# Optimization experiments

Hardware: AMD Instinct MI355X
Metric: run time of the kernel (lower is better)

The kernel has to match this reference:

```python
import jax, jax.numpy as jnp
import numpy as np

EPS = 1e-6
NUM_HEADS = 4


def setup_inputs() -> dict:
    key = jax.random.key(0)
    ks = jax.random.split(key, 7)
    B, C, H, W = 4, 128, 64, 64
    x = jax.random.normal(ks[0], (B, C, H, W), dtype=jnp.float32)
    norm_w = jnp.ones((C,), dtype=jnp.float32)
    norm_b = jnp.zeros((C,), dtype=jnp.float32)
    # 1x1 convs stored as [out_ch, in_ch] matrices
    qkv_w = jax.random.normal(ks[1], (3 * C, C), dtype=jnp.float32) / np.sqrt(C)
    qkv_b = jnp.zeros((3 * C,), dtype=jnp.float32)
    proj_w = jax.random.normal(ks[2], (C, C), dtype=jnp.float32) / np.sqrt(C)
    proj_b = jnp.zeros((C,), dtype=jnp.float32)
    return {"x": x, "norm_w": norm_w, "norm_b": norm_b,
            "qkv_w": qkv_w, "qkv_b": qkv_b, "proj_w": proj_w, "proj_b": proj_b}


def reference(x, norm_w, norm_b, qkv_w, qkv_b, proj_w, proj_b):
    B, C, H, W = x.shape
    nh = NUM_HEADS
    dh = C // nh
    N = H * W

    # ChannelLayerNorm: stats over channel dim per spatial position
    mean = jnp.mean(x, axis=1, keepdims=True)
    var = jnp.mean(jnp.square(x - mean), axis=1, keepdims=True)  # unbiased=False
    h = (x - mean) * jax.lax.rsqrt(var + EPS)
    h = h * norm_w[None, :, None, None] + norm_b[None, :, None, None]

    # qkv 1x1 conv -> [B, 3C, H, W]
    qkv = jnp.einsum('oc,bchw->bohw', qkv_w, h) + qkv_b[None, :, None, None]
    qkv = qkv.reshape(B, 3, nh, dh, N)
    q, k, v = qkv[:, 0], qkv[:, 1], qkv[:, 2]  # each [B, nh, dh, N]

    scale = dh ** -0.5
    attn = jnp.einsum('bhcn,bhcm->bhnm', q, k) * scale  # [B, nh, N, N]
    attn = jax.nn.softmax(attn, axis=-1)
    h = jnp.einsum('bhnm,bhcm->bhcn', attn, v)  # [B, nh, dh, N]
    h = h.reshape(B, C, H, W)

    h = jnp.einsum('oc,bchw->bohw', proj_w, h) + proj_b[None, :, None, None]
    return x + h
```

## Files before the change

### kernel.cpp

```cpp
#include <hip/hip_runtime.h>
#include <hip/hip_bf16.h>
#include <math.h>

#define BB 4
#define CC 128
#define NH 4
#define DH 32
#define NN 4096
#define OC3 (3*CC)

typedef __attribute__((ext_vector_type(8))) short short8;
typedef __attribute__((ext_vector_type(4))) short short4v;
typedef __attribute__((ext_vector_type(4))) float float4v;

__device__ inline short f2bf(float f) {
    unsigned u = __builtin_bit_cast(unsigned, f);
    u += 0x7FFF + ((u >> 16) & 1);
    return (short)(u >> 16);
}
__device__ inline unsigned pk2bf(float a, float b) {
    __hip_bfloat162 h = __float22bfloat162_rn(make_float2(a, b));
    unsigned u; __builtin_memcpy(&u, &h, 4);
    return u;
}

__global__ __launch_bounds__(256) void wcvt_kernel(
        const float* __restrict__ qw, const float* __restrict__ pw,
        short* __restrict__ wb) {
    int i = (blockIdx.x * 256 + threadIdx.x) * 8;
    const float* src = (i < OC3 * CC) ? (qw + i) : (pw + (i - OC3 * CC));
    float4 f0 = *(const float4*)(src);
    float4 f1 = *(const float4*)(src + 4);
    union { short8 v; unsigned u[4]; } z;
    z.u[0] = pk2bf(f0.x, f0.y); z.u[1] = pk2bf(f0.z, f0.w);
    z.u[2] = pk2bf(f1.x, f1.y); z.u[3] = pk2bf(f1.z, f1.w);
    *(short8*)(wb + i) = z.v;
}

#define HS 136
__global__ __launch_bounds__(512, 4) void lnqkv_kernel(
        const float* __restrict__ x, const float* __restrict__ nw,
        const float* __restrict__ nb, const short* __restrict__ qwb,
        const float* __restrict__ qbias,
        short* __restrict__ qT, short* __restrict__ kT, short* __restrict__ vv) {
    __shared__ short hT[64 * HS];
    __shared__ float red[16][64];
    __shared__ float mrs[2][64];
    int t = threadIdx.x;
    int n0g = blockIdx.x * 64;
    int b = n0g >> 12, n0 = n0g & (NN - 1);
    int nl = t & 63, cq = t >> 6;

    const float* xp = x + ((size_t)b * CC + cq * 16) * NN + n0 + nl;
    float xv[16];
    float s = 0.f, ss = 0.f;
    #pragma unroll
    for (int j = 0; j < 16; ++j) {
        xv[j] = xp[(size_t)j * NN];
        s += xv[j]; ss += xv[j] * xv[j];
    }
    red[cq][nl] = s; red[cq + 8][nl] = ss;
    __syncthreads();
    if (t < 64) {
        float s8 = 0.f, q8 = 0.f;
        #pragma unroll
        for (int j = 0; j < 8; ++j) { s8 += red[j][t]; q8 += red[j + 8][t]; }
        float mean = s8 * (1.0f / CC);
        float var  = q8 * (1.0f / CC) - mean * mean;
        mrs[0][t] = mean;
        mrs[1][t] = rsqrtf(var + 1e-6f);
    }
    __syncthreads();
    {
        float mean = mrs[0][nl], rsv = mrs[1][nl];
        #pragma unroll
        for (int j = 0; j < 16; j += 8) {
            union { short8 v; unsigned u[4]; } z;
            #pragma unroll
            for (int k = 0; k < 4; ++k) {
                int c = cq * 16 + j + 2 * k;
                float h0 = (xv[j + 2 * k]     - mean) * rsv * nw[c]     + nb[c];
                float h1 = (xv[j + 2 * k + 1] - mean) * rsv * nw[c + 1] + nb[c + 1];
                z.u[k] = pk2bf(h0, h1);
            }
            *(short8*)&hT[nl * HS + cq * 16 + j] = z.v;
        }
    }
    __syncthreads();

    int w = t >> 6, lane = t & 63;
    int lg = lane >> 4, ln = lane & 15;
    #pragma unroll
    for (int it = 0; it < 3; ++it) {
        int ow = (w + it * 8) * 16;
        const short* wp = qwb + (size_t)(ow + ln) * CC;
        float4v a0 = {0,0,0,0}, a1 = {0,0,0,0}, a2 = {0,0,0,0}, a3 = {0,0,0,0};
        #pragma unroll
        for (int cs = 0; cs < 4; ++cs) {
            short8 af = *(const short8*)(wp + cs * 32 + lg * 8);
            const short* hp = &hT[cs * 32 + lg * 8];
            a0 = __builtin_amdgcn_mfma_f32_16x16x32_bf16(af, *(const short8*)&hp[(0  + ln) * HS], a0, 0, 0, 0);
            a1 = __builtin_amdgcn_mfma_f32_16x16x32_bf16(af, *(const short8*)&hp[(16 + ln) * HS], a1, 0, 0, 0);
            a2 = __builtin_amdgcn_mfma_f32_16x16x32_bf16(af, *(const short8*)&hp[(32 + ln) * HS], a2, 0, 0, 0);
            a3 = __builtin_amdgcn_mfma_f32_16x16x32_bf16(af, *(const short8*)&hp[(48 + ln) * HS], a3, 0, 0, 0);
        }
        int r0 = ow + lg * 4;
        float b0 = qbias[r0], b1 = qbias[r0 + 1], b2 = qbias[r0 + 2], b3 = qbias[r0 + 3];
        int cb = ow & 31;
        float4v* accs[4] = {&a0, &a1, &a2, &a3};
        if (it == 0) {
            const float qs = 0.1767766952966369f * 1.4426950408889634f;
            int hh = ow >> 5;
            size_t rowbase = (size_t)(b * NH + hh) * NN + n0;
            #pragma unroll
            for (int nsub = 0; nsub < 4; ++nsub) {
                float4v av = *accs[nsub];
                union { short4v v; unsigned u[2]; } z;
                z.u[0] = pk2bf((av.x + b0) * qs, (av.y + b1) * qs);
                z.u[1] = pk2bf((av.z + b2) * qs, (av.w + b3) * qs);
                *(short4v*)&qT[(rowbase + nsub * 16 + ln) * DH + cb + lg * 4] = z.v;
            }
        } else if (it == 1) {
            int hh = (ow - CC) >> 5;
            size_t rowbase = (size_t)(b * NH + hh) * NN + n0;
            #pragma unroll
            for (int nsub = 0; nsub < 4; ++nsub) {
                float4v av = *accs[nsub];
                union { short4v v; unsigned u[2]; } z;
                z.u[0] = pk2bf(av.x + b0, av.y + b1);
                z.u[1] = pk2bf(av.z + b2, av.w + b3);
                *(short4v*)&kT[(rowbase + nsub * 16 + ln) * DH + cb + lg * 4] = z.v;
            }
        } else {
            int hh = (ow - 2 * CC) >> 5;
            size_t cbase = (size_t)((b * NH + hh) * DH + cb + lg * 4);
            #pragma unroll
            for (int nsub = 0; nsub < 4; ++nsub) {
                float4v av = *accs[nsub];
                size_t col = (size_t)n0 + nsub * 16 + ln;
                vv[(cbase + 0) * NN + col] = f2bf(av.x + b0);
                vv[(cbase + 1) * NN + col] = f2bf(av.y + b1);
                vv[(cbase + 2) * NN + col] = f2bf(av.z + b2);
                vv[(cbase + 3) * NN + col] = f2bf(av.w + b3);
            }
        }
    }
}

#define PS 72
union __align__(16) FlashSh {
    short pt[8 * 16 * PS];
    struct { float mo[3][8][64][8]; float ml[3][8][64]; } m;
};
__global__ __launch_bounds__(512, 2) void flash_kernel(
        const short* __restrict__ qT, const short* __restrict__ kT,
        const short* __restrict__ vv, short* __restrict__ aoT) {
    __shared__ FlashSh sh;
    int blk = blockIdx.x;
    int bh = blk >> 5;
    int qb = blk & 31;
    int b = bh >> 2, hh = bh & 3;
    int n0 = qb * 128;
    int t = threadIdx.x, w = t >> 6, lane = t & 63;
    int lg = lane >> 4, ln = lane & 15;
    int qg = w & 1;
    int split = w >> 1;

    const short* kbase = kT + (size_t)bh * NN * DH + lg * 8;
    const short* vb0 = vv + ((size_t)bh * DH + ln) * NN + lg * 8;
    const short* vb1 = vb0 + (size_t)16 * NN;

    short8 qf[4];
    #pragma unroll
    for (int j = 0; j < 4; ++j)
        qf[j] = *(const short8*)&qT[((size_t)bh * NN + n0 + (qg * 4 + j) * 16 + ln) * DH + lg * 8];

    union { short8 v; unsigned u[4]; } onesf;
    onesf.u[0] = 0x3F803F80u; onesf.u[1] = 0x3F803F80u;
    onesf.u[2] = 0x3F803F80u; onesf.u[3] = 0x3F803F80u;

    float4v o0[4], o1[4], sacc[4];
    #pragma unroll
    for (int j = 0; j < 4; ++j) {
        o0[j] = (float4v){0,0,0,0}; o1[j] = (float4v){0,0,0,0};
        sacc[j] = (float4v){0,0,0,0};
    }
    short* ptw = &sh.pt[w * 16 * PS];

    int mbeg = split * (NN / 4), mend = mbeg + NN / 4;
    for (int m0 = mbeg; m0 < mend; m0 += 64) {
        const short* kp = kbase + (size_t)m0 * DH;
        short8 k0 = *(const short8*)(kp + (size_t)(ln +  0) * DH);
        short8 k1 = *(const short8*)(kp + (size_t)(ln + 16) * DH);
        short8 k2 = *(const short8*)(kp + (size_t)(ln + 32) * DH);
        short8 k3 = *(const short8*)(kp + (size_t)(ln + 48) * DH);
        short8 v0 = *(const short8*)(vb0 + m0);
        short8 v1 = *(const short8*)(vb0 + m0 + 32);
        short8 v2 = *(const short8*)(vb1 + m0);
        short8 v3 = *(const short8*)(vb1 + m0 + 32);

        #pragma unroll
        for (int j = 0; j < 4; ++j) {
            float4v s0 = {0,0,0,0}, s1 = s0, s2 = s0, s3 = s0;
            s0 = __builtin_amdgcn_mfma_f32_16x16x32_bf16(k0, qf[j], s0, 0, 0, 0);
            s1 = __builtin_amdgcn_mfma_f32_16x16x32_bf16(k1, qf[j], s1, 0, 0, 0);
            s2 = __builtin_amdgcn_mfma_f32_16x16x32_bf16(k2, qf[j], s2, 0, 0, 0);
            s3 = __builtin_amdgcn_mfma_f32_16x16x32_bf16(k3, qf[j], s3, 0, 0, 0);
            float4v* sv[4] = {&s0, &s1, &s2, &s3};
            #pragma unroll
            for (int jj = 0; jj < 4; ++jj) {
                float4v sj = *sv[jj];
                float p0 = __builtin_amdgcn_exp2f(sj.x);
                float p1 = __builtin_amdgcn_exp2f(sj.y);
                float p2 = __builtin_amdgcn_exp2f(sj.z);
                float p3 = __builtin_amdgcn_exp2f(sj.w);
                union { short4v v; unsigned u[2]; } z;
                z.u[0] = pk2bf(p0, p1); z.u[1] = pk2bf(p2, p3);
                *(short4v*)&ptw[ln * PS + jj * 16 + lg * 4] = z.v;
            }
            short8 pb0 = *(const short8*)&ptw[ln * PS + 0  + lg * 8];
            short8 pb1 = *(const short8*)&ptw[ln * PS + 32 + lg * 8];
            o0[j]   = __builtin_amdgcn_mfma_f32_16x16x32_bf16(v0, pb0, o0[j], 0, 0, 0);
            o1[j]   = __builtin_amdgcn_mfma_f32_16x16x32_bf16(v2, pb0, o1[j], 0, 0, 0);
            sacc[j] = __builtin_amdgcn_mfma_f32_16x16x32_bf16(onesf.v, pb0, sacc[j], 0, 0, 0);
            o0[j]   = __builtin_amdgcn_mfma_f32_16x16x32_bf16(v1, pb1, o0[j], 0, 0, 0);
            o1[j]   = __builtin_amdgcn_mfma_f32_16x16x32_bf16(v3, pb1, o1[j], 0, 0, 0);
            sacc[j] = __builtin_amdgcn_mfma_f32_16x16x32_bf16(onesf.v, pb1, sacc[j], 0, 0, 0);
        }
    }

    float ls[4];
    #pragma unroll
    for (int j = 0; j < 4; ++j) ls[j] = sacc[j].x;

    __syncthreads();
    if (split > 0) {
        int si = split - 1;
        #pragma unroll
        for (int j = 0; j < 4; ++j) {
            int tid = qg * 4 + j;
            float* mp = &sh.m.mo[si][tid][lane][0];
            *(float4*)(mp + 0) = make_float4(o0[j].x, o0[j].y, o0[j].z, o0[j].w);
            *(float4*)(mp + 4) = make_float4(o1[j].x, o1[j].y, o1[j].z, o1[j].w);
            sh.m.ml[si][tid][lane] = ls[j];
        }
    }
    __syncthreads();
    if (split == 0) {
        #pragma unroll
        for (int j = 0; j < 4; ++j) {
            int tid = qg * 4 + j;
            #pragma unroll
            for (int si = 0; si < 3; ++si) {
                const float* mp = &sh.m.mo[si][tid][lane][0];
                float4 a0 = *(const float4*)(mp + 0);
                float4 a1 = *(const float4*)(mp + 4);
                o0[j].x += a0.x; o0[j].y += a0.y; o0[j].z += a0.z; o0[j].w += a0.w;
                o1[j].x += a1.x; o1[j].y += a1.y; o1[j].z += a1.z; o1[j].w += a1.w;
                ls[j] += sh.m.ml[si][tid][lane];
            }
            float inv = 1.0f / ls[j];
            short* ap = aoT + ((size_t)b * NN + n0 + tid * 16 + ln) * CC + hh * DH;
            union { short4v v; unsigned u[2]; } z;
            z.u[0] = pk2bf(o0[j].x * inv, o0[j].y * inv);
            z.u[1] = pk2bf(o0[j].z * inv, o0[j].w * inv);
            *(short4v*)&ap[lg * 4] = z.v;
            z.u[0] = pk2bf(o1[j].x * inv, o1[j].y * inv);
            z.u[1] = pk2bf(o1[j].z * inv, o1[j].w * inv);
            *(short4v*)&ap[16 + lg * 4] = z.v;
        }
    }
}

__global__ __launch_bounds__(256) void proj_kernel(
        const short* __restrict__ aoT, const short* __restrict__ pwb,
        const float* __restrict__ pb, const float* __restrict__ x,
        float* __restrict__ out) {
    int t = threadIdx.x;
    int n0g = blockIdx.x * 64;
    int b = n0g >> 12, n0 = n0g & (NN - 1);
    int o0 = blockIdx.y * 64;
    int wo = t >> 6, lane = t & 63;
    int lg = lane >> 4, ln = lane & 15;
    int ow = o0 + wo * 16;
    const short* wp = pwb + (size_t)(ow + ln) * CC;
    const short* ap = aoT + (size_t)n0g * CC + lg * 8;
    float4v a0 = {0,0,0,0}, a1 = {0,0,0,0}, a2 = {0,0,0,0}, a3 = {0,0,0,0};
    #pragma unroll
    for (int cs = 0; cs < 4; ++cs) {
        short8 af = *(const short8*)(wp + cs * 32 + lg * 8);
        const short* hp = ap + cs * 32;
        a0 = __builtin_amdgcn_mfma_f32_16x16x32_bf16(af, *(const short8*)&hp[(size_t)(0  + ln) * CC], a0, 0, 0, 0);
        a1 = __builtin_amdgcn_mfma_f32_16x16x32_bf16(af, *(const short8*)&hp[(size_t)(16 + ln) * CC], a1, 0, 0, 0);
        a2 = __builtin_amdgcn_mfma_f32_16x16x32_bf16(af, *(const short8*)&hp[(size_t)(32 + ln) * CC], a2, 0, 0, 0);
        a3 = __builtin_amdgcn_mfma_f32_16x16x32_bf16(af, *(const short8*)&hp[(size_t)(48 + ln) * CC], a3, 0, 0, 0);
    }
    int r0 = ow + lg * 4;
    float b0 = pb[r0], b1 = pb[r0 + 1], b2 = pb[r0 + 2], b3 = pb[r0 + 3];
    const float* xbase = x   + ((size_t)b * CC + r0) * NN + n0 + ln;
    float*       obase = out + ((size_t)b * CC + r0) * NN + n0 + ln;
    float4v* accs[4] = {&a0, &a1, &a2, &a3};
    #pragma unroll
    for (int nsub = 0; nsub < 4; ++nsub) {
        float4v av = *accs[nsub];
        const float* xp = xbase + nsub * 16;
        float* op = obase + nsub * 16;
        op[(size_t)0 * NN] = av.x + b0 + xp[(size_t)0 * NN];
        op[(size_t)1 * NN] = av.y + b1 + xp[(size_t)1 * NN];
        op[(size_t)2 * NN] = av.z + b2 + xp[(size_t)2 * NN];
        op[(size_t)3 * NN] = av.w + b3 + xp[(size_t)3 * NN];
    }
}

extern "C" void kernel_launch(void* const* d_in, const int* in_sizes, int n_in,
                              void* d_out, int out_size, void* d_ws, size_t ws_size,
                              hipStream_t stream) {
    const float* x    = (const float*)d_in[0];
    const float* nw   = (const float*)d_in[1];
    const float* nb   = (const float*)d_in[2];
    const float* qkvw = (const float*)d_in[3];
    const float* qkvb = (const float*)d_in[4];
    const float* pw   = (const float*)d_in[5];
    const float* pb   = (const float*)d_in[6];
    float* out = (float*)d_out;

    short* qT  = (short*)d_ws;
    short* kT  = qT + (size_t)BB * NH * NN * DH;
    short* vv  = kT + (size_t)BB * NH * NN * DH;
    short* aoT = vv + (size_t)BB * NH * DH * NN;
    short* wb  = aoT + (size_t)BB * NH * DH * NN;
    short* qwb = wb;
    short* pwb = wb + (size_t)OC3 * CC;

    wcvt_kernel<<<dim3(32), 256, 0, stream>>>(qkvw, pw, wb);
    lnqkv_kernel<<<dim3(256), 512, 0, stream>>>(x, nw, nb, qwb, qkvb, qT, kT, vv);
    flash_kernel<<<dim3(512), 512, 0, stream>>>(qT, kT, vv, aoT);
    proj_kernel<<<dim3(256, 2), 256, 0, stream>>>(aoT, pwb, pb, x, out);
}
```

Measured before the change: 153.5 us.

## Halve LN/proj tiles, prefetch K/V in flash loop, sum softmax denominators in VALU

New measurement: 153.5 us. Within noise of the previous version (-0.0%).

```diff
diff --git a/kernel.cpp b/kernel.cpp
--- a/kernel.cpp
+++ b/kernel.cpp
@@ -43,28 +43,28 @@
         const float* __restrict__ nb, const short* __restrict__ qwb,
         const float* __restrict__ qbias,
         short* __restrict__ qT, short* __restrict__ kT, short* __restrict__ vv) {
-    __shared__ short hT[64 * HS];
-    __shared__ float red[16][64];
-    __shared__ float mrs[2][64];
+    __shared__ short hT[32 * HS];
+    __shared__ float red[2][16][32];
+    __shared__ float mrs[2][32];
     int t = threadIdx.x;
-    int n0g = blockIdx.x * 64;
+    int n0g = blockIdx.x * 32;
     int b = n0g >> 12, n0 = n0g & (NN - 1);
-    int nl = t & 63, cq = t >> 6;
-
-    const float* xp = x + ((size_t)b * CC + cq * 16) * NN + n0 + nl;
-    float xv[16];
+    int nl = t & 31, cq = t >> 5;
+
+    const float* xp = x + ((size_t)b * CC + cq * 8) * NN + n0 + nl;
+    float xv[8];
     float s = 0.f, ss = 0.f;
     #pragma unroll
-    for (int j = 0; j < 16; ++j) {
+    for (int j = 0; j < 8; ++j) {
         xv[j] = xp[(size_t)j * NN];
         s += xv[j]; ss += xv[j] * xv[j];
     }
-    red[cq][nl] = s; red[cq + 8][nl] = ss;
-    __syncthreads();
-    if (t < 64) {
+    red[0][cq][nl] = s; red[1][cq][nl] = ss;
+    __syncthreads();
+    if (t < 32) {
         float s8 = 0.f, q8 = 0.f;
         #pragma unroll
-        for (int j = 0; j < 8; ++j) { s8 += red[j][t]; q8 += red[j + 8][t]; }
+        for (int j = 0; j < 16; ++j) { s8 += red[0][j][t]; q8 += red[1][j][t]; }
         float mean = s8 * (1.0f / CC);
         float var  = q8 * (1.0f / CC) - mean * mean;
         mrs[0][t] = mean;
@@ -73,18 +73,15 @@
     __syncthreads();
     {
         float mean = mrs[0][nl], rsv = mrs[1][nl];
-        #pragma unroll
-        for (int j = 0; j < 16; j += 8) {
-            union { short8 v; unsigned u[4]; } z;
-            #pragma unroll
-            for (int k = 0; k < 4; ++k) {
-                int c = cq * 16 + j + 2 * k;
-                float h0 = (xv[j + 2 * k]     - mean) * rsv * nw[c]     + nb[c];
-                float h1 = (xv[j + 2 * k + 1] - mean) * rsv * nw[c + 1] + nb[c + 1];
-                z.u[k] = pk2bf(h0, h1);
-            }
-            *(short8*)&hT[nl * HS + cq * 16 + j] = z.v;
-        }
+        union { short8 v; unsigned u[4]; } z;
+        #pragma unroll
+        for (int k = 0; k < 4; ++k) {
+            int c = cq * 8 + 2 * k;
+            float h0 = (xv[2 * k]     - mean) * rsv * nw[c]     + nb[c];
+            float h1 = (xv[2 * k + 1] - mean) * rsv * nw[c + 1] + nb[c + 1];
+            z.u[k] = pk2bf(h0, h1);
+        }
+        *(short8*)&hT[nl * HS + cq * 8] = z.v;
     }
     __syncthreads();
 
@@ -94,26 +91,24 @@
     for (int it = 0; it < 3; ++it) {
         int ow = (w + it * 8) * 16;
         const short* wp = qwb + (size_t)(ow + ln) * CC;
-        float4v a0 = {0,0,0,0}, a1 = {0,0,0,0}, a2 = {0,0,0,0}, a3 = {0,0,0,0};
+        float4v a0 = {0,0,0,0}, a1 = {0,0,0,0};
         #pragma unroll
         for (int cs = 0; cs < 4; ++cs) {
             short8 af = *(const short8*)(wp + cs * 32 + lg * 8);
             const short* hp = &hT[cs * 32 + lg * 8];
             a0 = __builtin_amdgcn_mfma_f32_16x16x32_bf16(af, *(const short8*)&hp[(0  + ln) * HS], a0, 0, 0, 0);
             a1 = __builtin_amdgcn_mfma_f32_16x16x32_bf16(af, *(const short8*)&hp[(16 + ln) * HS], a1, 0, 0, 0);
-            a2 = __builtin_amdgcn_mfma_f32_16x16x32_bf16(af, *(const short8*)&hp[(32 + ln) * HS], a2, 0, 0, 0);
-            a3 = __builtin_amdgcn_mfma_f32_16x16x32_bf16(af, *(const short8*)&hp[(48 + ln) * HS], a3, 0, 0, 0);
         }
         int r0 = ow + lg * 4;
         float b0 = qbias[r0], b1 = qbias[r0 + 1], b2 = qbias[r0 + 2], b3 = qbias[r0 + 3];
         int cb = ow & 31;
-        float4v* accs[4] = {&a0, &a1, &a2, &a3};
+        float4v* accs[2] = {&a0, &a1};
         if (it == 0) {
             const float qs = 0.1767766952966369f * 1.4426950408889634f;
             int hh = ow >> 5;
             size_t rowbase = (size_t)(b * NH + hh) * NN + n0;
             #pragma unroll
-            for (int nsub = 0; nsub < 4; ++nsub) {
+            for (int nsub = 0; nsub < 2; ++nsub) {
                 float4v av = *accs[nsub];
                 union { short4v v; unsigned u[2]; } z;
                 z.u[0] = pk2bf((av.x + b0) * qs, (av.y + b1) * qs);
@@ -124,7 +119,7 @@
             int hh = (ow - CC) >> 5;
             size_t rowbase = (size_t)(b * NH + hh) * NN + n0;
             #pragma unroll
-            for (int nsub = 0; nsub < 4; ++nsub) {
+            for (int nsub = 0; nsub < 2; ++nsub) {
                 float4v av = *accs[nsub];
                 union { short4v v; unsigned u[2]; } z;
                 z.u[0] = pk2bf(av.x + b0, av.y + b1);
@@ -135,7 +130,7 @@
             int hh = (ow - 2 * CC) >> 5;
             size_t cbase = (size_t)((b * NH + hh) * DH + cb + lg * 4);
             #pragma unroll
-            for (int nsub = 0; nsub < 4; ++nsub) {
+            for (int nsub = 0; nsub < 2; ++nsub) {
                 float4v av = *accs[nsub];
                 size_t col = (size_t)n0 + nsub * 16 + ln;
                 vv[(cbase + 0) * NN + col] = f2bf(av.x + b0);
@@ -175,29 +170,37 @@
     for (int j = 0; j < 4; ++j)
         qf[j] = *(const short8*)&qT[((size_t)bh * NN + n0 + (qg * 4 + j) * 16 + ln) * DH + lg * 8];
 
-    union { short8 v; unsigned u[4]; } onesf;
-    onesf.u[0] = 0x3F803F80u; onesf.u[1] = 0x3F803F80u;
-    onesf.u[2] = 0x3F803F80u; onesf.u[3] = 0x3F803F80u;
-
-    float4v o0[4], o1[4], sacc[4];
+    float4v o0[4], o1[4];
+    float ls[4];
     #pragma unroll
     for (int j = 0; j < 4; ++j) {
-        o0[j] = (float4v){0,0,0,0}; o1[j] = (float4v){0,0,0,0};
-        sacc[j] = (float4v){0,0,0,0};
+        o0[j] = (float4v){0,0,0,0}; o1[j] = (float4v){0,0,0,0}; ls[j] = 0.f;
     }
     short* ptw = &sh.pt[w * 16 * PS];
 
     int mbeg = split * (NN / 4), mend = mbeg + NN / 4;
+
+    const short* kp0 = kbase + (size_t)mbeg * DH;
+    short8 k0 = *(const short8*)(kp0 + (size_t)(ln +  0) * DH);
+    short8 k1 = *(const short8*)(kp0 + (size_t)(ln + 16) * DH);
+    short8 k2 = *(const short8*)(kp0 + (size_t)(ln + 32) * DH);
+    short8 k3 = *(const short8*)(kp0 + (size_t)(ln + 48) * DH);
+    short8 v0 = *(const short8*)(vb0 + mbeg);
+    short8 v1 = *(const short8*)(vb0 + mbeg + 32);
+    short8 v2 = *(const short8*)(vb1 + mbeg);
+    short8 v3 = *(const short8*)(vb1 + mbeg + 32);
+
     for (int m0 = mbeg; m0 < mend; m0 += 64) {
-        const short* kp = kbase + (size_t)m0 * DH;
-        short8 k0 = *(const short8*)(kp + (size_t)(ln +  0) * DH);
-        short8 k1 = *(const short8*)(kp + (size_t)(ln + 16) * DH);
-        short8 k2 = *(const short8*)(kp + (size_t)(ln + 32) * DH);
-        short8 k3 = *(const short8*)(kp + (size_t)(ln + 48) * DH);
-        short8 v0 = *(const short8*)(vb0 + m0);
-        short8 v1 = *(const short8*)(vb0 + m0 + 32);
-        short8 v2 = *(const short8*)(vb1 + m0);
-        short8 v3 = *(const short8*)(vb1 + m0 + 32);
+        int mn = (m0 + 64 < mend) ? m0 + 64 : mbeg;
+        const short* kpn = kbase + (size_t)mn * DH;
+        short8 kn0 = *(const short8*)(kpn + (size_t)(ln +  0) * DH);
+        short8 kn1 = *(const short8*)(kpn + (size_t)(ln + 16) * DH);
+        short8 kn2 = *(const short8*)(kpn + (size_t)(ln + 32) * DH);
+        short8 kn3 = *(const short8*)(kpn + (size_t)(ln + 48) * DH);
+        short8 vn0 = *(const short8*)(vb0 + mn);
+        short8 vn1 = *(const short8*)(vb0 + mn + 32);
+        short8 vn2 = *(const short8*)(vb1 + mn);
+        short8 vn3 = *(const short8*)(vb1 + mn + 32);
 
         #pragma unroll
         for (int j = 0; j < 4; ++j) {
@@ -206,6 +209,7 @@
             s1 = __builtin_amdgcn_mfma_f32_16x16x32_bf16(k1, qf[j], s1, 0, 0, 0);
             s2 = __builtin_amdgcn_mfma_f32_16x16x32_bf16(k2, qf[j], s2, 0, 0, 0);
             s3 = __builtin_amdgcn_mfma_f32_16x16x32_bf16(k3, qf[j], s3, 0, 0, 0);
+            float lacc = 0.f;
             float4v* sv[4] = {&s0, &s1, &s2, &s3};
             #pragma unroll
             for (int jj = 0; jj < 4; ++jj) {
@@ -214,24 +218,23 @@
                 float p1 = __builtin_amdgcn_exp2f(sj.y);
                 float p2 = __builtin_amdgcn_exp2f(sj.z);
                 float p3 = __builtin_amdgcn_exp2f(sj.w);
+                lacc += (p0 + p1) + (p2 + p3);
                 union { short4v v; unsigned u[2]; } z;
                 z.u[0] = pk2bf(p0, p1); z.u[1] = pk2bf(p2, p3);
                 *(short4v*)&ptw[ln * PS + jj * 16 + lg * 4] = z.v;
             }
+            ls[j] += lacc;
             short8 pb0 = *(const short8*)&ptw[ln * PS + 0  + lg * 8];
             short8 pb1 = *(const short8*)&ptw[ln * PS + 32 + lg * 8];
-            o0[j]   = __builtin_amdgcn_mfma_f32_16x16x32_bf16(v0, pb0, o0[j], 0, 0, 0);
-            o1[j]   = __builtin_amdgcn_mfma_f32_16x16x32_bf16(v2, pb0, o1[j], 0, 0, 0);
-            sacc[j] = __builtin_amdgcn_mfma_f32_16x16x32_bf16(onesf.v, pb0, sacc[j], 0, 0, 0);
-            o0[j]   = __builtin_amdgcn_mfma_f32_16x16x32_bf16(v1, pb1, o0[j], 0, 0, 0);
-            o1[j]   = __builtin_amdgcn_mfma_f32_16x16x32_bf16(v3, pb1, o1[j], 0, 0, 0);
-            sacc[j] = __builtin_amdgcn_mfma_f32_16x16x32_bf16(onesf.v, pb1, sacc[j], 0, 0, 0);
-        }
-    }
-
-    float ls[4];
-    #pragma unroll
-    for (int j = 0; j < 4; ++j) ls[j] = sacc[j].x;
+            o0[j] = __builtin_amdgcn_mfma_f32_16x16x32_bf16(v0, pb0, o0[j], 0, 0, 0);
+            o1[j] = __builtin_amdgcn_mfma_f32_16x16x32_bf16(v2, pb0, o1[j], 0, 0, 0);
+            o0[j] = __builtin_amdgcn_mfma_f32_16x16x32_bf16(v1, pb1, o0[j], 0, 0, 0);
+            o1[j] = __builtin_amdgcn_mfma_f32_16x16x32_bf16(v3, pb1, o1[j], 0, 0, 0);
+        }
+
+        k0 = kn0; k1 = kn1; k2 = kn2; k3 = kn3;
+        v0 = vn0; v1 = vn1; v2 = vn2; v3 = vn3;
+    }
 
     __syncthreads();
     if (split > 0) {
@@ -259,7 +262,10 @@
                 o1[j].x += a1.x; o1[j].y += a1.y; o1[j].z += a1.z; o1[j].w += a1.w;
                 ls[j] += sh.m.ml[si][tid][lane];
             }
-            float inv = 1.0f / ls[j];
+            float lt = ls[j];
+            lt += __shfl_xor(lt, 16, 64);
+            lt += __shfl_xor(lt, 32, 64);
+            float inv = 1.0f / lt;
             short* ap = aoT + ((size_t)b * NN + n0 + tid * 16 + ln) * CC + hh * DH;
             union { short4v v; unsigned u[2]; } z;
             z.u[0] = pk2bf(o0[j].x * inv, o0[j].y * inv);
@@ -277,7 +283,7 @@
         const float* __restrict__ pb, const float* __restrict__ x,
         float* __restrict__ out) {
     int t = threadIdx.x;
-    int n0g = blockIdx.x * 64;
+    int n0g = blockIdx.x * 32;
     int b = n0g >> 12, n0 = n0g & (NN - 1);
     int o0 = blockIdx.y * 64;
     int wo = t >> 6, lane = t & 63;
@@ -285,23 +291,21 @@
     int ow = o0 + wo * 16;
     const short* wp = pwb + (size_t)(ow + ln) * CC;
     const short* ap = aoT + (size_t)n0g * CC + lg * 8;
-    float4v a0 = {0,0,0,0}, a1 = {0,0,0,0}, a2 = {0,0,0,0}, a3 = {0,0,0,0};
+    float4v a0 = {0,0,0,0}, a1 = {0,0,0,0};
     #pragma unroll
     for (int cs = 0; cs < 4; ++cs) {
         short8 af = *(const short8*)(wp + cs * 32 + lg * 8);
         const short* hp = ap + cs * 32;
         a0 = __builtin_amdgcn_mfma_f32_16x16x32_bf16(af, *(const short8*)&hp[(size_t)(0  + ln) * CC], a0, 0, 0, 0);
         a1 = __builtin_amdgcn_mfma_f32_16x16x32_bf16(af, *(const short8*)&hp[(size_t)(16 + ln) * CC], a1, 0, 0, 0);
-        a2 = __builtin_amdgcn_mfma_f32_16x16x32_bf16(af, *(const short8*)&hp[(size_t)(32 + ln) * CC], a2, 0, 0, 0);
-        a3 = __builtin_amdgcn_mfma_f32_16x16x32_bf16(af, *(const short8*)&hp[(size_t)(48 + ln) * CC], a3, 0, 0, 0);
     }
     int r0 = ow + lg * 4;
     float b0 = pb[r0], b1 = pb[r0 + 1], b2 = pb[r0 + 2], b3 = pb[r0 + 3];
     const float* xbase = x   + ((size_t)b * CC + r0) * NN + n0 + ln;
     float*       obase = out + ((size_t)b * CC + r0) * NN + n0 + ln;
-    float4v* accs[4] = {&a0, &a1, &a2, &a3};
-    #pragma unroll
-    for (int nsub = 0; nsub < 4; ++nsub) {
+    float4v* accs[2] = {&a0, &a1};
+    #pragma unroll
+    for (int nsub = 0; nsub < 2; ++nsub) {
         float4v av = *accs[nsub];
         const float* xp = xbase + nsub * 16;
         float* op = obase + nsub * 16;
@@ -333,7 +337,7 @@
     short* pwb = wb + (size_t)OC3 * CC;
 
     wcvt_kernel<<<dim3(32), 256, 0, stream>>>(qkvw, pw, wb);
-    lnqkv_kernel<<<dim3(256), 512, 0, stream>>>(x, nw, nb, qwb, qkvb, qT, kT, vv);
+    lnqkv_kernel<<<dim3(512), 512, 0, stream>>>(x, nw, nb, qwb, qkvb, qT, kT, vv);
     flash_kernel<<<dim3(512), 512, 0, stream>>>(qT, kT, vv, aoT);
-    proj_kernel<<<dim3(256, 2), 256, 0, stream>>>(aoT, pwb, pb, x, out);
-}
+    proj_kernel<<<dim3(512, 2), 256, 0, stream>>>(aoT, pwb, pb, x, out);
+}
```

## Vectorize LN loads and proj epilogue; compute softmax row sums on VALU

Applied to the files above, without the earlier changes.

After: 148.0 us. -3.6%, faster.

```diff
diff --git a/kernel.cpp b/kernel.cpp
--- a/kernel.cpp
+++ b/kernel.cpp
@@ -44,27 +44,36 @@
         const float* __restrict__ qbias,
         short* __restrict__ qT, short* __restrict__ kT, short* __restrict__ vv) {
     __shared__ short hT[64 * HS];
-    __shared__ float red[16][64];
+    __shared__ float red[2][32][68];
     __shared__ float mrs[2][64];
     int t = threadIdx.x;
     int n0g = blockIdx.x * 64;
     int b = n0g >> 12, n0 = n0g & (NN - 1);
-    int nl = t & 63, cq = t >> 6;
-
-    const float* xp = x + ((size_t)b * CC + cq * 16) * NN + n0 + nl;
-    float xv[16];
-    float s = 0.f, ss = 0.f;
-    #pragma unroll
-    for (int j = 0; j < 16; ++j) {
-        xv[j] = xp[(size_t)j * NN];
-        s += xv[j]; ss += xv[j] * xv[j];
-    }
-    red[cq][nl] = s; red[cq + 8][nl] = ss;
+    int nq = t & 15;
+    int cg = t >> 4;
+
+    const float* xb = x + ((size_t)b * CC + cg * 4) * NN + n0 + nq * 4;
+    float xe[4][4];
+    {
+        float s0 = 0.f, s1 = 0.f, s2 = 0.f, s3 = 0.f;
+        float q0 = 0.f, q1 = 0.f, q2 = 0.f, q3 = 0.f;
+        #pragma unroll
+        for (int c = 0; c < 4; ++c) {
+            float4 v = *(const float4*)(xb + (size_t)c * NN);
+            xe[c][0] = v.x; xe[c][1] = v.y; xe[c][2] = v.z; xe[c][3] = v.w;
+            s0 += v.x; q0 += v.x * v.x;
+            s1 += v.y; q1 += v.y * v.y;
+            s2 += v.z; q2 += v.z * v.z;
+            s3 += v.w; q3 += v.w * v.w;
+        }
+        *(float4*)&red[0][cg][nq * 4] = make_float4(s0, s1, s2, s3);
+        *(float4*)&red[1][cg][nq * 4] = make_float4(q0, q1, q2, q3);
+    }
     __syncthreads();
     if (t < 64) {
         float s8 = 0.f, q8 = 0.f;
         #pragma unroll
-        for (int j = 0; j < 8; ++j) { s8 += red[j][t]; q8 += red[j + 8][t]; }
+        for (int j = 0; j < 32; ++j) { s8 += red[0][j][t]; q8 += red[1][j][t]; }
         float mean = s8 * (1.0f / CC);
         float var  = q8 * (1.0f / CC) - mean * mean;
         mrs[0][t] = mean;
@@ -72,18 +81,20 @@
     }
     __syncthreads();
     {
-        float mean = mrs[0][nl], rsv = mrs[1][nl];
-        #pragma unroll
-        for (int j = 0; j < 16; j += 8) {
-            union { short8 v; unsigned u[4]; } z;
-            #pragma unroll
-            for (int k = 0; k < 4; ++k) {
-                int c = cq * 16 + j + 2 * k;
-                float h0 = (xv[j + 2 * k]     - mean) * rsv * nw[c]     + nb[c];
-                float h1 = (xv[j + 2 * k + 1] - mean) * rsv * nw[c + 1] + nb[c + 1];
-                z.u[k] = pk2bf(h0, h1);
-            }
-            *(short8*)&hT[nl * HS + cq * 16 + j] = z.v;
+        int c0 = cg * 4;
+        float w0 = nw[c0], w1 = nw[c0 + 1], w2 = nw[c0 + 2], w3 = nw[c0 + 3];
+        float e0 = nb[c0], e1 = nb[c0 + 1], e2 = nb[c0 + 2], e3 = nb[c0 + 3];
+        #pragma unroll
+        for (int k = 0; k < 4; ++k) {
+            int token = nq * 4 + k;
+            float m = mrs[0][token], r = mrs[1][token];
+            float h0 = (xe[0][k] - m) * r * w0 + e0;
+            float h1 = (xe[1][k] - m) * r * w1 + e1;
+            float h2 = (xe[2][k] - m) * r * w2 + e2;
+            float h3 = (xe[3][k] - m) * r * w3 + e3;
+            union { short4v v; unsigned u[2]; } z;
+            z.u[0] = pk2bf(h0, h1); z.u[1] = pk2bf(h2, h3);
+            *(short4v*)&hT[token * HS + c0] = z.v;
         }
     }
     __syncthreads();
@@ -175,15 +186,11 @@
     for (int j = 0; j < 4; ++j)
         qf[j] = *(const short8*)&qT[((size_t)bh * NN + n0 + (qg * 4 + j) * 16 + ln) * DH + lg * 8];
 
-    union { short8 v; unsigned u[4]; } onesf;
-    onesf.u[0] = 0x3F803F80u; onesf.u[1] = 0x3F803F80u;
-    onesf.u[2] = 0x3F803F80u; onesf.u[3] = 0x3F803F80u;
-
-    float4v o0[4], o1[4], sacc[4];
+    float4v o0[4], o1[4];
+    float ls[4];
     #pragma unroll
     for (int j = 0; j < 4; ++j) {
-        o0[j] = (float4v){0,0,0,0}; o1[j] = (float4v){0,0,0,0};
-        sacc[j] = (float4v){0,0,0,0};
+        o0[j] = (float4v){0,0,0,0}; o1[j] = (float4v){0,0,0,0}; ls[j] = 0.f;
     }
     short* ptw = &sh.pt[w * 16 * PS];
 
@@ -206,6 +213,7 @@
             s1 = __builtin_amdgcn_mfma_f32_16x16x32_bf16(k1, qf[j], s1, 0, 0, 0);
             s2 = __builtin_amdgcn_mfma_f32_16x16x32_bf16(k2, qf[j], s2, 0, 0, 0);
             s3 = __builtin_amdgcn_mfma_f32_16x16x32_bf16(k3, qf[j], s3, 0, 0, 0);
+            float lacc = 0.f;
             float4v* sv[4] = {&s0, &s1, &s2, &s3};
             #pragma unroll
             for (int jj = 0; jj < 4; ++jj) {
@@ -214,24 +222,20 @@
                 float p1 = __builtin_amdgcn_exp2f(sj.y);
                 float p2 = __builtin_amdgcn_exp2f(sj.z);
                 float p3 = __builtin_amdgcn_exp2f(sj.w);
+                lacc += (p0 + p1) + (p2 + p3);
                 union { short4v v; unsigned u[2]; } z;
                 z.u[0] = pk2bf(p0, p1); z.u[1] = pk2bf(p2, p3);
                 *(short4v*)&ptw[ln * PS + jj * 16 + lg * 4] = z.v;
             }
+            ls[j] += lacc;
             short8 pb0 = *(const short8*)&ptw[ln * PS + 0  + lg * 8];
             short8 pb1 = *(const short8*)&ptw[ln * PS + 32 + lg * 8];
-            o0[j]   = __builtin_amdgcn_mfma_f32_16x16x32_bf16(v0, pb0, o0[j], 0, 0, 0);
-            o1[j]   = __builtin_amdgcn_mfma_f32_16x16x32_bf16(v2, pb0, o1[j], 0, 0, 0);
-            sacc[j] = __builtin_amdgcn_mfma_f32_16x16x32_bf16(onesf.v, pb0, sacc[j], 0, 0, 0);
-            o0[j]   = __builtin_amdgcn_mfma_f32_16x16x32_bf16(v1, pb1, o0[j], 0, 0, 0);
-            o1[j]   = __builtin_amdgcn_mfma_f32_16x16x32_bf16(v3, pb1, o1[j], 0, 0, 0);
-            sacc[j] = __builtin_amdgcn_mfma_f32_16x16x32_bf16(onesf.v, pb1, sacc[j], 0, 0, 0);
-        }
-    }
-
-    float ls[4];
-    #pragma unroll
-    for (int j = 0; j < 4; ++j) ls[j] = sacc[j].x;
+            o0[j] = __builtin_amdgcn_mfma_f32_16x16x32_bf16(v0, pb0, o0[j], 0, 0, 0);
+            o1[j] = __builtin_amdgcn_mfma_f32_16x16x32_bf16(v2, pb0, o1[j], 0, 0, 0);
+            o0[j] = __builtin_amdgcn_mfma_f32_16x16x32_bf16(v1, pb1, o0[j], 0, 0, 0);
+            o1[j] = __builtin_amdgcn_mfma_f32_16x16x32_bf16(v3, pb1, o1[j], 0, 0, 0);
+        }
+    }
 
     __syncthreads();
     if (split > 0) {
@@ -259,7 +263,10 @@
                 o1[j].x += a1.x; o1[j].y += a1.y; o1[j].z += a1.z; o1[j].w += a1.w;
                 ls[j] += sh.m.ml[si][tid][lane];
             }
-            float inv = 1.0f / ls[j];
+            float lt = ls[j];
+            lt += __shfl_xor(lt, 16, 64);
+            lt += __shfl_xor(lt, 32, 64);
+            float inv = 1.0f / lt;
             short* ap = aoT + ((size_t)b * NN + n0 + tid * 16 + ln) * CC + hh * DH;
             union { short4v v; unsigned u[2]; } z;
             z.u[0] = pk2bf(o0[j].x * inv, o0[j].y * inv);
@@ -276,6 +283,7 @@
         const short* __restrict__ aoT, const short* __restrict__ pwb,
         const float* __restrict__ pb, const float* __restrict__ x,
         float* __restrict__ out) {
+    __shared__ float ot[64][68];
     int t = threadIdx.x;
     int n0g = blockIdx.x * 64;
     int b = n0g >> 12, n0 = n0g & (NN - 1);
@@ -295,20 +303,34 @@
         a2 = __builtin_amdgcn_mfma_f32_16x16x32_bf16(af, *(const short8*)&hp[(size_t)(32 + ln) * CC], a2, 0, 0, 0);
         a3 = __builtin_amdgcn_mfma_f32_16x16x32_bf16(af, *(const short8*)&hp[(size_t)(48 + ln) * CC], a3, 0, 0, 0);
     }
-    int r0 = ow + lg * 4;
-    float b0 = pb[r0], b1 = pb[r0 + 1], b2 = pb[r0 + 2], b3 = pb[r0 + 3];
-    const float* xbase = x   + ((size_t)b * CC + r0) * NN + n0 + ln;
-    float*       obase = out + ((size_t)b * CC + r0) * NN + n0 + ln;
-    float4v* accs[4] = {&a0, &a1, &a2, &a3};
-    #pragma unroll
-    for (int nsub = 0; nsub < 4; ++nsub) {
-        float4v av = *accs[nsub];
-        const float* xp = xbase + nsub * 16;
-        float* op = obase + nsub * 16;
-        op[(size_t)0 * NN] = av.x + b0 + xp[(size_t)0 * NN];
-        op[(size_t)1 * NN] = av.y + b1 + xp[(size_t)1 * NN];
-        op[(size_t)2 * NN] = av.z + b2 + xp[(size_t)2 * NN];
-        op[(size_t)3 * NN] = av.w + b3 + xp[(size_t)3 * NN];
+    {
+        int chb = wo * 16 + lg * 4;
+        float4v* accs[4] = {&a0, &a1, &a2, &a3};
+        #pragma unroll
+        for (int nsub = 0; nsub < 4; ++nsub) {
+            float4v av = *accs[nsub];
+            int tok = nsub * 16 + ln;
+            ot[chb + 0][tok] = av.x;
+            ot[chb + 1][tok] = av.y;
+            ot[chb + 2][tok] = av.z;
+            ot[chb + 3][tok] = av.w;
+        }
+    }
+    __syncthreads();
+    {
+        int tq = t & 15, cg = t >> 4;
+        #pragma unroll
+        for (int i = 0; i < 4; ++i) {
+            int chl = cg + i * 16;
+            int chg = o0 + chl;
+            float4 o4 = *(const float4*)&ot[chl][tq * 4];
+            float bias = pb[chg];
+            const float* xp = x + ((size_t)b * CC + chg) * NN + n0 + tq * 4;
+            float*       op = out + ((size_t)b * CC + chg) * NN + n0 + tq * 4;
+            float4 xr = *(const float4*)xp;
+            *(float4*)op = make_float4(o4.x + bias + xr.x, o4.y + bias + xr.y,
+                                       o4.z + bias + xr.z, o4.w + bias + xr.w);
+        }
     }
 }
 
```
